# Kernel optimization log

Measured on AMD Instinct MI355X. Metric: run time of the kernel, lower is better.

## Reference

```python
import jax, jax.numpy as jnp
import numpy as np

BETA = 0.5
TAU_L = 0.1
TAU_H = 0.1
TOP_K = 2


def setup_inputs() -> dict:
    key = jax.random.key(0)
    ks = jax.random.split(key, 6)
    B, S, H, F, E, NH = 1, 2048, 1024, 3584, 8, 16
    hidden_states = jax.random.normal(ks[0], (B, S, H), dtype=jnp.float32)
    self_attn_weights = jax.random.uniform(ks[1], (B, NH, S, S), dtype=jnp.float32)
    gate_w = jax.random.normal(ks[2], (E, H), dtype=jnp.float32) * 0.02
    w1 = jax.random.normal(ks[3], (E, F, H), dtype=jnp.float32) * 0.02
    w2 = jax.random.normal(ks[4], (E, H, F), dtype=jnp.float32) * 0.02
    w3 = jax.random.normal(ks[5], (E, F, H), dtype=jnp.float32) * 0.02
    return {"hidden_states": hidden_states, "self_attn_weights": self_attn_weights,
            "gate_w": gate_w, "w1": w1, "w2": w2, "w3": w3}


def reference(hidden_states, self_attn_weights, gate_w, w1, w2, w3):
    B, S, H = hidden_states.shape
    E = gate_w.shape[0]
    x = hidden_states.reshape(-1, H)          # [T, H], T = B*S
    T = x.shape[0]

    router_logits = x @ gate_w.T              # [T, E]
    rw_full = jax.nn.softmax(router_logits.astype(jnp.float32), axis=-1)
    rw, sel = jax.lax.top_k(rw_full, TOP_K)   # [T, 2]

    # --- dynamic pruning branch (loss_index < block_range) ---
    mask_top1 = rw[:, 1] < BETA * rw[:, 0]
    new_routing = jnp.ones_like(rw)
    new_routing = new_routing.at[:, 1].set(jnp.where(mask_top1, 0.0, 1.0))

    # sequence_length > 1: attention-based token pruning (assumes B == 1)
    mean_tensor = jnp.mean(jnp.squeeze(self_attn_weights), axis=0)  # [S, S]
    column = mean_tensor.shape[1]
    real_number = jnp.arange(column, 0, -1, dtype=jnp.float32)
    attention_scores = jnp.sum(mean_tensor, axis=1) / real_number   # [S]
    l1_norm = jnp.sum(jnp.abs(x), axis=1)                           # [T]
    attention_scores = attention_scores * l1_norm

    n_low = int(TAU_L * T)
    n_high = int(TAU_H * T)
    _, low_idx = jax.lax.top_k(-attention_scores, n_low)   # smallest
    _, high_idx = jax.lax.top_k(attention_scores, n_high)  # largest
    mask_all = jnp.zeros((T,), dtype=bool).at[low_idx].set(True)
    keep_all = jnp.zeros((T,), dtype=bool).at[high_idx].set(True)
    new_routing = jnp.where(mask_all[:, None], 0.0, new_routing)
    new_routing = jnp.where(keep_all[:, None], 1.0, new_routing)

    rw = rw * new_routing
    denom = jnp.sum(rw, axis=-1, keepdims=True)
    rw = rw / jnp.where(denom > 0, denom, 1.0)  # fully-masked tokens -> 0 output
    rw = rw.astype(x.dtype)

    # combine weights per (token, expert); dispatch mask == new_routing
    cw = jnp.sum(rw[:, :, None] * jax.nn.one_hot(sel, E, dtype=rw.dtype), axis=1)  # [T, E]

    # dense reference for the gather-expert-scatter loop (SwiGLU experts)
    h = jnp.einsum('th,efh->tef', x, w1)      # [T, E, F]
    g = jnp.einsum('th,efh->tef', x, w3)
    a = jax.nn.silu(h) * g
    y = jnp.einsum('tef,ehf->teh', a, w2)     # [T, E, H]
    out = jnp.einsum('te,teh->th', cw, y)     # [T, H]

    return out.reshape(B, S, H), router_logits
```

## Files before the change

kernel.cpp:

```cpp
#include <hip/hip_runtime.h>
#include <hip/hip_bf16.h>
#include <math.h>

#define NTOK 2048
#define HDIM 1024
#define NEXP 8
#define FDIM 3584
#define NHEADS 16
#define NLOW 204
#define NHIGH 204
#define BK 32
#define LDST 40

typedef __bf16 bf16x8 __attribute__((ext_vector_type(8)));
typedef float f32x4 __attribute__((ext_vector_type(4)));

__global__ __launch_bounds__(256) void k_router(
    const float* __restrict__ x, const float* __restrict__ gw,
    float* __restrict__ logits, float* __restrict__ l1,
    int* __restrict__ sel0, int* __restrict__ sel1,
    float* __restrict__ rw0, float* __restrict__ rw1)
{
    __shared__ float sgw[NEXP * HDIM];
    int tid = threadIdx.x;
    for (int i = tid; i < NEXP * HDIM; i += 256) sgw[i] = gw[i];
    __syncthreads();
    int wv = tid >> 6, lane = tid & 63;
    int t = blockIdx.x * 4 + wv;
    const float* xr = x + (size_t)t * HDIM;
    float acc[NEXP];
#pragma unroll
    for (int e = 0; e < NEXP; ++e) acc[e] = 0.f;
    float al1 = 0.f;
    for (int h = lane; h < HDIM; h += 64) {
        float xv = xr[h];
        al1 += fabsf(xv);
#pragma unroll
        for (int e = 0; e < NEXP; ++e) acc[e] += xv * sgw[e * HDIM + h];
    }
#pragma unroll
    for (int off = 32; off > 0; off >>= 1) {
#pragma unroll
        for (int e = 0; e < NEXP; ++e) acc[e] += __shfl_xor(acc[e], off);
        al1 += __shfl_xor(al1, off);
    }
    if (lane < NEXP) logits[t * NEXP + lane] = acc[lane];
    if (lane == 0) {
        l1[t] = al1;
        float m = acc[0];
#pragma unroll
        for (int e = 1; e < NEXP; ++e) m = fmaxf(m, acc[e]);
        float p[NEXP], s = 0.f;
#pragma unroll
        for (int e = 0; e < NEXP; ++e) { p[e] = expf(acc[e] - m); s += p[e]; }
        float inv = 1.f / s;
        float b0 = -1.f, b1 = -1.f; int i0 = 0, i1 = 0;
#pragma unroll
        for (int e = 0; e < NEXP; ++e) {
            float r = p[e] * inv;
            if (r > b0) { b1 = b0; i1 = i0; b0 = r; i0 = e; }
            else if (r > b1) { b1 = r; i1 = e; }
        }
        sel0[t] = i0; sel1[t] = i1; rw0[t] = b0; rw1[t] = b1;
    }
}

__global__ __launch_bounds__(256) void k_attn(
    const float* __restrict__ attn, const float* __restrict__ l1,
    float* __restrict__ scores)
{
    int i = blockIdx.x, tid = threadIdx.x;
    float acc = 0.f;
    for (int h = 0; h < NHEADS; ++h) {
        const float4* p = (const float4*)(attn + ((size_t)h * NTOK + i) * NTOK);
        for (int j = tid; j < NTOK / 4; j += 256) {
            float4 v = p[j];
            acc += v.x + v.y + v.z + v.w;
        }
    }
    __shared__ float red[256];
    red[tid] = acc; __syncthreads();
    for (int s = 128; s > 0; s >>= 1) {
        if (tid < s) red[tid] += red[tid + s];
        __syncthreads();
    }
    if (tid == 0) scores[i] = red[0] / (16.f * (float)(NTOK - i)) * l1[i];
}

__global__ __launch_bounds__(256) void k_rank(
    const float* __restrict__ scores, const float* __restrict__ rw0,
    const float* __restrict__ rw1, float* __restrict__ w0f, float* __restrict__ w1f)
{
    __shared__ float s[NTOK];
    int tid = threadIdx.x;
    for (int i = tid; i < NTOK; i += 256) s[i] = scores[i];
    __syncthreads();
    int t = blockIdx.x * 256 + tid;
    float st = s[t];
    int cl = 0, ch = 0;
    for (int j = 0; j < NTOK; ++j) {
        float sj = s[j];
        int tie = (sj == st) && (j < t);
        cl += (sj < st) || tie;
        ch += (sj > st) || tie;
    }
    bool in_low = cl < NLOW, keep = ch < NHIGH;
    float a = rw0[t], b = rw1[t];
    float n0 = 1.f, n1 = (b < 0.5f * a) ? 0.f : 1.f;
    if (in_low) { n0 = 0.f; n1 = 0.f; }
    if (keep)   { n0 = 1.f; n1 = 1.f; }
    a *= n0; b *= n1;
    float d = a + b;
    if (d > 0.f) { a /= d; b /= d; }
    w0f[t] = a; w1f[t] = b;
}

__global__ __launch_bounds__(512) void k_build(
    const int* __restrict__ sel0, const int* __restrict__ sel1,
    const float* __restrict__ w0f, const float* __restrict__ w1f,
    int* __restrict__ tok, float* __restrict__ wgt,
    int* __restrict__ counts, int* __restrict__ offs)
{
    int tid = threadIdx.x;
    int e = tid >> 6, lane = tid & 63;
    unsigned long long below = (1ull << lane) - 1ull;
    int base = 0;
    for (int r = 0; r < NTOK / 64; ++r) {
        int t = r * 64 + lane;
        bool f0 = (sel0[t] == e) && (w0f[t] > 0.f);
        unsigned long long m0 = __ballot(f0);
        if (f0) {
            int pos = base + __popcll(m0 & below);
            tok[e * NTOK + pos] = t; wgt[e * NTOK + pos] = w0f[t];
        }
        base += __popcll(m0);
        bool f1 = (sel1[t] == e) && (w1f[t] > 0.f);
        unsigned long long m1 = __ballot(f1);
        if (f1) {
            int pos = base + __popcll(m1 & below);
            tok[e * NTOK + pos] = t; wgt[e * NTOK + pos] = w1f[t];
        }
        base += __popcll(m1);
    }
    if (lane == 0) counts[e] = base;
    __syncthreads();
    if (tid == 0) {
        int o = 0;
        for (int i = 0; i < NEXP; ++i) { offs[i] = o; o += counts[i]; }
    }
}

__global__ __launch_bounds__(256) void k_zero(float4* __restrict__ out)
{
    out[blockIdx.x * 256 + threadIdx.x] = make_float4(0.f, 0.f, 0.f, 0.f);
}

__device__ inline void stage8(__hip_bfloat16* dst, const float* src)
{
    float4 a = *(const float4*)src;
    float4 b = *(const float4*)(src + 4);
    bf16x8 v;
    v[0] = (__bf16)a.x; v[1] = (__bf16)a.y; v[2] = (__bf16)a.z; v[3] = (__bf16)a.w;
    v[4] = (__bf16)b.x; v[5] = (__bf16)b.y; v[6] = (__bf16)b.z; v[7] = (__bf16)b.w;
    *(bf16x8*)dst = v;
}

__global__ __launch_bounds__(256) void k_ffn1(
    const float* __restrict__ x, const float* __restrict__ w1,
    const float* __restrict__ w3,
    const int* __restrict__ tok, const float* __restrict__ wgt,
    const int* __restrict__ counts, const int* __restrict__ offs,
    __hip_bfloat16* __restrict__ act)
{
    int e = blockIdx.z;
    int cnt = counts[e];
    int m0 = blockIdx.y * 64;
    if (m0 >= cnt) return;
    int f0 = blockIdx.x * 64;
    int tid = threadIdx.x;
    __shared__ __hip_bfloat16 sX[64 * LDST], sW1[64 * LDST], sW3[64 * LDST];
    __shared__ int sTok[64];
    __shared__ float sWgt[64];
    if (tid < 64) {
        int row = m0 + tid;
        int rr = (row < cnt) ? row : (cnt - 1);
        sTok[tid] = tok[e * NTOK + rr];
        sWgt[tid] = (row < cnt) ? wgt[e * NTOK + row] : 0.f;
    }
    __syncthreads();

    int r = tid >> 2, kk = (tid & 3) * 8;
    const float* xp  = x  + (size_t)sTok[r] * HDIM + kk;
    const float* w1p = w1 + ((size_t)e * FDIM + f0 + r) * HDIM + kk;
    const float* w3p = w3 + ((size_t)e * FDIM + f0 + r) * HDIM + kk;

    int wv = tid >> 6, lane = tid & 63;
    f32x4 acc1[4] = {}, acc3[4] = {};
    const int rowA = wv * 16 + (lane & 15);
    const int kfrag = (lane >> 4) * 8;

    for (int k0 = 0; k0 < HDIM; k0 += BK) {
        stage8(&sX[r * LDST + kk], xp + k0);
        stage8(&sW1[r * LDST + kk], w1p + k0);
        stage8(&sW3[r * LDST + kk], w3p + k0);
        __syncthreads();
        bf16x8 a = *(const bf16x8*)&sX[rowA * LDST + kfrag];
#pragma unroll
        for (int c = 0; c < 4; ++c) {
            bf16x8 b1 = *(const bf16x8*)&sW1[(c * 16 + (lane & 15)) * LDST + kfrag];
            acc1[c] = __builtin_amdgcn_mfma_f32_16x16x32_bf16(a, b1, acc1[c], 0, 0, 0);
            bf16x8 b3 = *(const bf16x8*)&sW3[(c * 16 + (lane & 15)) * LDST + kfrag];
            acc3[c] = __builtin_amdgcn_mfma_f32_16x16x32_bf16(a, b3, acc3[c], 0, 0, 0);
        }
        __syncthreads();
    }
    int soff = offs[e];
#pragma unroll
    for (int c = 0; c < 4; ++c) {
#pragma unroll
        for (int rr = 0; rr < 4; ++rr) {
            int rloc = wv * 16 + (lane >> 4) * 4 + rr;
            if (m0 + rloc < cnt) {
                float hv = acc1[c][rr], gv = acc3[c][rr];
                float av = hv / (1.f + expf(-hv)) * gv * sWgt[rloc];
                act[(size_t)(soff + m0 + rloc) * FDIM + f0 + c * 16 + (lane & 15)] =
                    (__hip_bfloat16)av;
            }
        }
    }
}

__global__ __launch_bounds__(256) void k_ffn2(
    const __hip_bfloat16* __restrict__ act, const float* __restrict__ w2,
    const int* __restrict__ tok, const int* __restrict__ counts,
    const int* __restrict__ offs, float* __restrict__ out)
{
    int e = blockIdx.z;
    int cnt = counts[e];
    int m0 = blockIdx.y * 64;
    if (m0 >= cnt) return;
    int h0 = blockIdx.x * 64;
    int tid = threadIdx.x;
    __shared__ __hip_bfloat16 sA[64 * LDST], sB[64 * LDST];
    __shared__ int sTok[64];
    if (tid < 64) {
        int row = m0 + tid;
        sTok[tid] = (row < cnt) ? tok[e * NTOK + row] : 0;
    }
    __syncthreads();
    int soff = offs[e];
    int r = tid >> 2, kk = (tid & 3) * 8;
    int arow = (m0 + r < cnt) ? (m0 + r) : (cnt - 1);
    const __hip_bfloat16* ap = act + (size_t)(soff + arow) * FDIM + kk;
    const float* bp = w2 + ((size_t)e * HDIM + h0 + r) * FDIM + kk;
    int wv = tid >> 6, lane = tid & 63;
    f32x4 acc[4] = {};
    const int rowA = wv * 16 + (lane & 15);
    const int kfrag = (lane >> 4) * 8;
    for (int k0 = 0; k0 < FDIM; k0 += BK) {
        *(bf16x8*)&sA[r * LDST + kk] = *(const bf16x8*)(ap + k0);
        stage8(&sB[r * LDST + kk], bp + k0);
        __syncthreads();
        bf16x8 a = *(const bf16x8*)&sA[rowA * LDST + kfrag];
#pragma unroll
        for (int c = 0; c < 4; ++c) {
            bf16x8 b = *(const bf16x8*)&sB[(c * 16 + (lane & 15)) * LDST + kfrag];
            acc[c] = __builtin_amdgcn_mfma_f32_16x16x32_bf16(a, b, acc[c], 0, 0, 0);
        }
        __syncthreads();
    }
#pragma unroll
    for (int c = 0; c < 4; ++c) {
#pragma unroll
        for (int rr2 = 0; rr2 < 4; ++rr2) {
            int rloc = wv * 16 + (lane >> 4) * 4 + rr2;
            if (m0 + rloc < cnt) {
                int t = sTok[rloc];
                atomicAdd(&out[(size_t)t * HDIM + h0 + c * 16 + (lane & 15)], acc[c][rr2]);
            }
        }
    }
}

extern "C" void kernel_launch(void* const* d_in, const int* in_sizes, int n_in,
                              void* d_out, int out_size, void* d_ws, size_t ws_size,
                              hipStream_t stream)
{
    const float* x    = (const float*)d_in[0];
    const float* attn = (const float*)d_in[1];
    const float* gw   = (const float*)d_in[2];
    const float* w1   = (const float*)d_in[3];
    const float* w2   = (const float*)d_in[4];
    const float* w3   = (const float*)d_in[5];
    float* out = (float*)d_out;
    float* logits = out + (size_t)NTOK * HDIM;

    char* ws = (char*)d_ws;
    float* l1     = (float*)(ws + 0);
    float* scores = (float*)(ws + 8192);
    int*   sel0   = (int*)(ws + 16384);
    int*   sel1   = (int*)(ws + 24576);
    float* rw0    = (float*)(ws + 32768);
    float* rw1    = (float*)(ws + 40960);
    float* w0f    = (float*)(ws + 49152);
    float* w1f    = (float*)(ws + 57344);
    int*   counts = (int*)(ws + 65536);
    int*   offs   = (int*)(ws + 65600);
    int*   tok    = (int*)(ws + 73728);
    float* wgt    = (float*)(ws + 143360);
    __hip_bfloat16* act = (__hip_bfloat16*)(ws + 1048576);

    k_router<<<NTOK / 4, 256, 0, stream>>>(x, gw, logits, l1, sel0, sel1, rw0, rw1);
    k_attn<<<NTOK, 256, 0, stream>>>(attn, l1, scores);
    k_rank<<<NEXP, 256, 0, stream>>>(scores, rw0, rw1, w0f, w1f);
    k_build<<<1, 512, 0, stream>>>(sel0, sel1, w0f, w1f, tok, wgt, counts, offs);
    k_zero<<<NTOK, 256, 0, stream>>>((float4*)out);
    k_ffn1<<<dim3(FDIM / 64, NTOK / 64, NEXP), 256, 0, stream>>>(
        x, w1, w3, tok, wgt, counts, offs, act);
    k_ffn2<<<dim3(HDIM / 64, NTOK / 64, NEXP), 256, 0, stream>>>(
        act, w2, tok, counts, offs, out);
}
```

Baseline: 477.0 us.

## Enlarge FFN GEMM tiles to 128x128 with double-buffered register-prefetched LDS staging

Both expert GEMM kernels move from 64x64 to 128x128 block tiles, with each wave computing a 64x64 sub-tile (4x4 MFMA fragments) instead of 16x64. The next K-slice is prefetched into registers and written to a second LDS buffer while the MFMAs run, so only one barrier is needed per iteration. The aim is better operand reuse, less global and LDS traffic per FLOP, and overlap of loads with compute. In exchange, register pressure rises sharply (acc1/acc3 take 128 accumulator floats in ffn1), and the larger tiles give fewer blocks and more wasted work on partially filled expert tiles.

After: 488.7 us. 1.02x slower.

```diff
diff --git a/kernel.cpp b/kernel.cpp
--- a/kernel.cpp
+++ b/kernel.cpp
@@ -155,17 +155,28 @@
     out[blockIdx.x * 256 + threadIdx.x] = make_float4(0.f, 0.f, 0.f, 0.f);
 }
 
-__device__ inline void stage8(__hip_bfloat16* dst, const float* src)
-{
-    float4 a = *(const float4*)src;
-    float4 b = *(const float4*)(src + 4);
-    bf16x8 v;
-    v[0] = (__bf16)a.x; v[1] = (__bf16)a.y; v[2] = (__bf16)a.z; v[3] = (__bf16)a.w;
-    v[4] = (__bf16)b.x; v[5] = (__bf16)b.y; v[6] = (__bf16)b.z; v[7] = (__bf16)b.w;
-    *(bf16x8*)dst = v;
-}
-
-__global__ __launch_bounds__(256) void k_ffn1(
+struct F16v { float4 a, b, c, d; };
+__device__ inline F16v ld16(const float* __restrict__ p)
+{
+    F16v v;
+    v.a = *(const float4*)p;
+    v.b = *(const float4*)(p + 4);
+    v.c = *(const float4*)(p + 8);
+    v.d = *(const float4*)(p + 12);
+    return v;
+}
+__device__ inline void st16(__hip_bfloat16* dst, const F16v& v)
+{
+    bf16x8 lo, hi;
+    lo[0] = (__bf16)v.a.x; lo[1] = (__bf16)v.a.y; lo[2] = (__bf16)v.a.z; lo[3] = (__bf16)v.a.w;
+    lo[4] = (__bf16)v.b.x; lo[5] = (__bf16)v.b.y; lo[6] = (__bf16)v.b.z; lo[7] = (__bf16)v.b.w;
+    hi[0] = (__bf16)v.c.x; hi[1] = (__bf16)v.c.y; hi[2] = (__bf16)v.c.z; hi[3] = (__bf16)v.c.w;
+    hi[4] = (__bf16)v.d.x; hi[5] = (__bf16)v.d.y; hi[6] = (__bf16)v.d.z; hi[7] = (__bf16)v.d.w;
+    *(bf16x8*)dst = lo;
+    *(bf16x8*)(dst + 8) = hi;
+}
+
+__global__ __launch_bounds__(256, 2) void k_ffn1(
     const float* __restrict__ x, const float* __restrict__ w1,
     const float* __restrict__ w3,
     const int* __restrict__ tok, const float* __restrict__ wgt,
@@ -174,14 +185,16 @@
 {
     int e = blockIdx.z;
     int cnt = counts[e];
-    int m0 = blockIdx.y * 64;
+    int m0 = blockIdx.y * 128;
     if (m0 >= cnt) return;
-    int f0 = blockIdx.x * 64;
-    int tid = threadIdx.x;
-    __shared__ __hip_bfloat16 sX[64 * LDST], sW1[64 * LDST], sW3[64 * LDST];
-    __shared__ int sTok[64];
-    __shared__ float sWgt[64];
-    if (tid < 64) {
+    int f0 = blockIdx.x * 128;
+    int tid = threadIdx.x;
+    __shared__ __align__(16) __hip_bfloat16 sX[2][128 * LDST];
+    __shared__ __align__(16) __hip_bfloat16 sW1[2][128 * LDST];
+    __shared__ __align__(16) __hip_bfloat16 sW3[2][128 * LDST];
+    __shared__ int sTok[128];
+    __shared__ float sWgt[128];
+    if (tid < 128) {
         int row = m0 + tid;
         int rr = (row < cnt) ? row : (cnt - 1);
         sTok[tid] = tok[e * NTOK + rr];
@@ -189,94 +202,148 @@
     }
     __syncthreads();
 
-    int r = tid >> 2, kk = (tid & 3) * 8;
-    const float* xp  = x  + (size_t)sTok[r] * HDIM + kk;
-    const float* w1p = w1 + ((size_t)e * FDIM + f0 + r) * HDIM + kk;
-    const float* w3p = w3 + ((size_t)e * FDIM + f0 + r) * HDIM + kk;
+    int r = tid >> 1, c16 = (tid & 1) * 16;
+    const float* xp  = x  + (size_t)sTok[r] * HDIM + c16;
+    const float* w1p = w1 + ((size_t)e * FDIM + f0 + r) * HDIM + c16;
+    const float* w3p = w3 + ((size_t)e * FDIM + f0 + r) * HDIM + c16;
+    int sidx = r * LDST + c16;
+
+    F16v va = ld16(xp), vb = ld16(w1p), vc = ld16(w3p);
+    st16(&sX[0][sidx], va); st16(&sW1[0][sidx], vb); st16(&sW3[0][sidx], vc);
+    __syncthreads();
 
     int wv = tid >> 6, lane = tid & 63;
-    f32x4 acc1[4] = {}, acc3[4] = {};
-    const int rowA = wv * 16 + (lane & 15);
-    const int kfrag = (lane >> 4) * 8;
-
+    int wm = (wv >> 1) * 64, wf = (wv & 1) * 64;
+    int col = lane & 15, kfrag = (lane >> 4) * 8;
+    f32x4 acc1[4][4] = {}, acc3[4][4] = {};
+    int cur = 0;
     for (int k0 = 0; k0 < HDIM; k0 += BK) {
-        stage8(&sX[r * LDST + kk], xp + k0);
-        stage8(&sW1[r * LDST + kk], w1p + k0);
-        stage8(&sW3[r * LDST + kk], w3p + k0);
+        bool more = (k0 + BK) < HDIM;
+        if (more) {
+            va = ld16(xp + k0 + BK);
+            vb = ld16(w1p + k0 + BK);
+            vc = ld16(w3p + k0 + BK);
+        }
+        bf16x8 af[4], b1[4], b3[4];
+#pragma unroll
+        for (int m = 0; m < 4; ++m)
+            af[m] = *(const bf16x8*)&sX[cur][(wm + m * 16 + col) * LDST + kfrag];
+#pragma unroll
+        for (int f = 0; f < 4; ++f) {
+            b1[f] = *(const bf16x8*)&sW1[cur][(wf + f * 16 + col) * LDST + kfrag];
+            b3[f] = *(const bf16x8*)&sW3[cur][(wf + f * 16 + col) * LDST + kfrag];
+        }
+#pragma unroll
+        for (int m = 0; m < 4; ++m)
+#pragma unroll
+            for (int f = 0; f < 4; ++f) {
+                acc1[m][f] = __builtin_amdgcn_mfma_f32_16x16x32_bf16(af[m], b1[f], acc1[m][f], 0, 0, 0);
+                acc3[m][f] = __builtin_amdgcn_mfma_f32_16x16x32_bf16(af[m], b3[f], acc3[m][f], 0, 0, 0);
+            }
+        if (more) {
+            st16(&sX[cur ^ 1][sidx], va);
+            st16(&sW1[cur ^ 1][sidx], vb);
+            st16(&sW3[cur ^ 1][sidx], vc);
+        }
         __syncthreads();
-        bf16x8 a = *(const bf16x8*)&sX[rowA * LDST + kfrag];
-#pragma unroll
-        for (int c = 0; c < 4; ++c) {
-            bf16x8 b1 = *(const bf16x8*)&sW1[(c * 16 + (lane & 15)) * LDST + kfrag];
-            acc1[c] = __builtin_amdgcn_mfma_f32_16x16x32_bf16(a, b1, acc1[c], 0, 0, 0);
-            bf16x8 b3 = *(const bf16x8*)&sW3[(c * 16 + (lane & 15)) * LDST + kfrag];
-            acc3[c] = __builtin_amdgcn_mfma_f32_16x16x32_bf16(a, b3, acc3[c], 0, 0, 0);
-        }
-        __syncthreads();
+        cur ^= 1;
     }
     int soff = offs[e];
 #pragma unroll
-    for (int c = 0; c < 4; ++c) {
-#pragma unroll
-        for (int rr = 0; rr < 4; ++rr) {
-            int rloc = wv * 16 + (lane >> 4) * 4 + rr;
+    for (int m = 0; m < 4; ++m) {
+        int mb = wm + m * 16 + (lane >> 4) * 4;
+#pragma unroll
+        for (int q = 0; q < 4; ++q) {
+            int rloc = mb + q;
             if (m0 + rloc < cnt) {
-                float hv = acc1[c][rr], gv = acc3[c][rr];
-                float av = hv / (1.f + expf(-hv)) * gv * sWgt[rloc];
-                act[(size_t)(soff + m0 + rloc) * FDIM + f0 + c * 16 + (lane & 15)] =
-                    (__hip_bfloat16)av;
+                float wgtv = sWgt[rloc];
+#pragma unroll
+                for (int f = 0; f < 4; ++f) {
+                    float hv = acc1[m][f][q], gv = acc3[m][f][q];
+                    float av = hv / (1.f + expf(-hv)) * gv * wgtv;
+                    act[(size_t)(soff + m0 + rloc) * FDIM + f0 + wf + f * 16 + col] =
+                        (__hip_bfloat16)av;
+                }
             }
         }
     }
 }
 
-__global__ __launch_bounds__(256) void k_ffn2(
+__global__ __launch_bounds__(256, 3) void k_ffn2(
     const __hip_bfloat16* __restrict__ act, const float* __restrict__ w2,
     const int* __restrict__ tok, const int* __restrict__ counts,
     const int* __restrict__ offs, float* __restrict__ out)
 {
     int e = blockIdx.z;
     int cnt = counts[e];
-    int m0 = blockIdx.y * 64;
+    int m0 = blockIdx.y * 128;
     if (m0 >= cnt) return;
-    int h0 = blockIdx.x * 64;
-    int tid = threadIdx.x;
-    __shared__ __hip_bfloat16 sA[64 * LDST], sB[64 * LDST];
-    __shared__ int sTok[64];
-    if (tid < 64) {
+    int h0 = blockIdx.x * 128;
+    int tid = threadIdx.x;
+    __shared__ __align__(16) __hip_bfloat16 sA[2][128 * LDST];
+    __shared__ __align__(16) __hip_bfloat16 sB[2][128 * LDST];
+    __shared__ int sTok[128];
+    if (tid < 128) {
         int row = m0 + tid;
         sTok[tid] = (row < cnt) ? tok[e * NTOK + row] : 0;
     }
     __syncthreads();
     int soff = offs[e];
-    int r = tid >> 2, kk = (tid & 3) * 8;
+    int r = tid >> 1, c16 = (tid & 1) * 16;
     int arow = (m0 + r < cnt) ? (m0 + r) : (cnt - 1);
-    const __hip_bfloat16* ap = act + (size_t)(soff + arow) * FDIM + kk;
-    const float* bp = w2 + ((size_t)e * HDIM + h0 + r) * FDIM + kk;
+    const __hip_bfloat16* ap = act + (size_t)(soff + arow) * FDIM + c16;
+    const float* bp = w2 + ((size_t)e * HDIM + h0 + r) * FDIM + c16;
+    int sidx = r * LDST + c16;
+
+    bf16x8 a0 = *(const bf16x8*)ap, a1 = *(const bf16x8*)(ap + 8);
+    F16v vb = ld16(bp);
+    *(bf16x8*)&sA[0][sidx] = a0; *(bf16x8*)&sA[0][sidx + 8] = a1;
+    st16(&sB[0][sidx], vb);
+    __syncthreads();
+
     int wv = tid >> 6, lane = tid & 63;
-    f32x4 acc[4] = {};
-    const int rowA = wv * 16 + (lane & 15);
-    const int kfrag = (lane >> 4) * 8;
+    int wm = (wv >> 1) * 64, wh = (wv & 1) * 64;
+    int col = lane & 15, kfrag = (lane >> 4) * 8;
+    f32x4 acc[4][4] = {};
+    int cur = 0;
     for (int k0 = 0; k0 < FDIM; k0 += BK) {
-        *(bf16x8*)&sA[r * LDST + kk] = *(const bf16x8*)(ap + k0);
-        stage8(&sB[r * LDST + kk], bp + k0);
+        bool more = (k0 + BK) < FDIM;
+        if (more) {
+            a0 = *(const bf16x8*)(ap + k0 + BK);
+            a1 = *(const bf16x8*)(ap + k0 + BK + 8);
+            vb = ld16(bp + k0 + BK);
+        }
+        bf16x8 aa[4], bb[4];
+#pragma unroll
+        for (int m = 0; m < 4; ++m)
+            aa[m] = *(const bf16x8*)&sA[cur][(wm + m * 16 + col) * LDST + kfrag];
+#pragma unroll
+        for (int f = 0; f < 4; ++f)
+            bb[f] = *(const bf16x8*)&sB[cur][(wh + f * 16 + col) * LDST + kfrag];
+#pragma unroll
+        for (int m = 0; m < 4; ++m)
+#pragma unroll
+            for (int f = 0; f < 4; ++f)
+                acc[m][f] = __builtin_amdgcn_mfma_f32_16x16x32_bf16(aa[m], bb[f], acc[m][f], 0, 0, 0);
+        if (more) {
+            *(bf16x8*)&sA[cur ^ 1][sidx] = a0;
+            *(bf16x8*)&sA[cur ^ 1][sidx + 8] = a1;
+            st16(&sB[cur ^ 1][sidx], vb);
+        }
         __syncthreads();
-        bf16x8 a = *(const bf16x8*)&sA[rowA * LDST + kfrag];
-#pragma unroll
-        for (int c = 0; c < 4; ++c) {
-            bf16x8 b = *(const bf16x8*)&sB[(c * 16 + (lane & 15)) * LDST + kfrag];
-            acc[c] = __builtin_amdgcn_mfma_f32_16x16x32_bf16(a, b, acc[c], 0, 0, 0);
-        }
-        __syncthreads();
-    }
-#pragma unroll
-    for (int c = 0; c < 4; ++c) {
-#pragma unroll
-        for (int rr2 = 0; rr2 < 4; ++rr2) {
-            int rloc = wv * 16 + (lane >> 4) * 4 + rr2;
+        cur ^= 1;
+    }
+#pragma unroll
+    for (int m = 0; m < 4; ++m) {
+        int mb = wm + m * 16 + (lane >> 4) * 4;
+#pragma unroll
+        for (int q = 0; q < 4; ++q) {
+            int rloc = mb + q;
             if (m0 + rloc < cnt) {
                 int t = sTok[rloc];
-                atomicAdd(&out[(size_t)t * HDIM + h0 + c * 16 + (lane & 15)], acc[c][rr2]);
+#pragma unroll
+                for (int f = 0; f < 4; ++f)
+                    atomicAdd(&out[(size_t)t * HDIM + h0 + wh + f * 16 + col], acc[m][f][q]);
             }
         }
     }
@@ -315,8 +382,8 @@
     k_rank<<<NEXP, 256, 0, stream>>>(scores, rw0, rw1, w0f, w1f);
     k_build<<<1, 512, 0, stream>>>(sel0, sel1, w0f, w1f, tok, wgt, counts, offs);
     k_zero<<<NTOK, 256, 0, stream>>>((float4*)out);
-    k_ffn1<<<dim3(FDIM / 64, NTOK / 64, NEXP), 256, 0, stream>>>(
+    k_ffn1<<<dim3(FDIM / 128, NTOK / 128, NEXP), 256, 0, stream>>>(
         x, w1, w3, tok, wgt, counts, offs, act);
-    k_ffn2<<<dim3(HDIM / 64, NTOK / 64, NEXP), 256, 0, stream>>>(
+    k_ffn2<<<dim3(HDIM / 128, NTOK / 128, NEXP), 256, 0, stream>>>(
         act, w2, tok, counts, offs, out);
 }
```
